# Performance work log

Hardware: AMD Instinct MI355X
Metric: run time of the kernel (lower is better)

## Reference

```python
import jax, jax.numpy as jnp
import numpy as np

B = 8192
D_IN = 2048
MM = 1600
CHUNKS = 20
CS = MM // CHUNKS  # 80
D_OUT = 3000
EPS = 1e-12  # F.normalize clamp eps


def setup_inputs() -> dict:
    key = jax.random.key(0)
    ks = jax.random.split(key, 10)
    s_in = 1.0 / np.sqrt(D_IN)
    s_c = 1.0 / np.sqrt(CS)
    s_mm = 1.0 / np.sqrt(MM)
    return {
        "x0": jax.random.normal(ks[0], (B, D_IN), jnp.float32),
        "x1": jax.random.normal(ks[1], (B, D_IN), jnp.float32),
        "W0": jax.random.uniform(ks[2], (D_IN, MM), jnp.float32, -s_in, s_in),
        "b0": jax.random.uniform(ks[3], (MM,), jnp.float32, -s_in, s_in),
        "W1": jax.random.uniform(ks[4], (D_IN, MM), jnp.float32, -s_in, s_in),
        "b1": jax.random.uniform(ks[5], (MM,), jnp.float32, -s_in, s_in),
        # stacked bilinear weights: [chunks, out, in1, in2] like torch Bilinear
        "Wb": jax.random.uniform(ks[6], (CHUNKS, CS, CS, CS), jnp.float32, -s_c, s_c),
        "bb": jax.random.uniform(ks[7], (CHUNKS, CS), jnp.float32, -s_c, s_c),
        "Wout": jax.random.uniform(ks[8], (MM, D_OUT), jnp.float32, -s_mm, s_mm),
        "bout": jax.random.uniform(ks[9], (D_OUT,), jnp.float32, -s_mm, s_mm),
    }


def reference(x0, x1, W0, b0, W1, b1, Wb, bb, Wout, bout):
    # input projections: [B, MM]
    h0 = x0 @ W0 + b0
    h1 = x1 @ W1 + b1
    # split into equal chunks: [B, CHUNKS, CS]
    h0c = h0.reshape(B, CHUNKS, CS)
    h1c = h1.reshape(B, CHUNKS, CS)
    # batched bilinear over all chunks: z[b,c,o] = sum_{s,t} h0[b,c,s] Wb[c,o,s,t] h1[b,c,t] + bb[c,o]
    z = jnp.einsum('bcs,cost,bct->bco', h0c, Wb, h1c) + bb[None, :, :]
    # signed sqrt (pos_norm == 'before_cat')
    z = jnp.sqrt(jax.nn.relu(z)) - jnp.sqrt(jax.nn.relu(-z))
    # L2 normalize per chunk (torch F.normalize over dim=1 of the [B, CS] chunk)
    norm = jnp.linalg.norm(z, axis=-1, keepdims=True)
    z = z / jnp.maximum(norm, EPS)
    # concat chunks -> [B, MM], final projection
    z = z.reshape(B, MM)
    return z @ Wout + bout
```

## Files before the change

kernel.cpp:

```cpp
#include <hip/hip_runtime.h>
#include <hip/hip_bf16.h>

typedef unsigned short u16;
typedef unsigned int   u32;

using bf16x8 = __attribute__((ext_vector_type(8))) short;
using f32x4  = __attribute__((ext_vector_type(4))) float;
using fvec4  = __attribute__((ext_vector_type(4))) float;
using u16x4  = __attribute__((ext_vector_type(4))) unsigned short;

#define BSZ   8192
#define DIN   2048
#define MMD   1600
#define NCH   20
#define CSZ   80
#define DOUT  3000

__device__ __forceinline__ float bf2f(u16 u) {
    u32 x = ((u32)u) << 16; float f; __builtin_memcpy(&f, &x, 4); return f;
}
__device__ __forceinline__ u16 f2bf(float f) {
    u32 x; __builtin_memcpy(&x, &f, 4);
    u32 r = x + 0x7fffu + ((x >> 16) & 1u);
    return (u16)(r >> 16);
}

__device__ __forceinline__ void gl2lds16(const void* g, const void* l) {
    __builtin_amdgcn_global_load_lds(
        (const __attribute__((address_space(1))) u32*)g,
        (__attribute__((address_space(3))) u32*)l, 16, 0, 0);
}

__global__ void cast_bf16_k(const float* __restrict__ src, u16* __restrict__ dst, int n4) {
    int i = blockIdx.x * blockDim.x + threadIdx.x;
    if (i < n4) {
        fvec4 v = ((const fvec4*)src)[i];
        u16x4 o;
        o.x = f2bf(v.x); o.y = f2bf(v.y); o.z = f2bf(v.z); o.w = f2bf(v.w);
        ((u16x4*)dst)[i] = o;
    }
}

__global__ void transpose_cast_k(const float* __restrict__ src, u16* __restrict__ dst,
                                 int K, int N) {
    __shared__ float t[32][33];
    int k0 = blockIdx.x * 32, n0 = blockIdx.y * 32;
    int tx = threadIdx.x & 31, ty = threadIdx.x >> 5;
#pragma unroll
    for (int r = 0; r < 4; r++) {
        int n = n0 + tx;
        float v = (n < N) ? src[(size_t)(k0 + ty + 8 * r) * N + n] : 0.f;
        t[ty + 8 * r][tx] = v;
    }
    __syncthreads();
#pragma unroll
    for (int r = 0; r < 4; r++)
        dst[(size_t)(n0 + ty + 8 * r) * K + k0 + tx] = f2bf(t[tx][ty + 8 * r]);
}

template<bool OUT_BF16>
__global__ __launch_bounds__(256, 2) void gemm_bt_k(
    const u16* __restrict__ A, const u16* __restrict__ BT,
    const float* __restrict__ bias, void* __restrict__ C, int K, int N) {
    __shared__ __align__(16) u16 As[128 * 64];
    __shared__ __align__(16) u16 Bs[128 * 64];
    const int tid = threadIdx.x, w = tid >> 6, lane = tid & 63;
    const int lr = lane & 15, lk = lane >> 4, s7 = lr & 7;
    const int m0 = blockIdx.x * 128, n0 = blockIdx.y * 128;
    const int mh = (w >> 1) * 64, nh = (w & 1) * 64;
    const int so = (lane & 7) ^ (lane >> 3);
    int arow[4], brow[4];
#pragma unroll
    for (int i = 0; i < 4; i++) { arow[i] = (mh + i * 16 + lr) * 64; brow[i] = (nh + i * 16 + lr) * 64; }
    f32x4 acc[4][4] = {};
    const u16* Ag = A + (size_t)m0 * K;
    const u16* Bg = BT + (size_t)n0 * K;
    const int nslab = K >> 6;
    for (int kt = 0; kt < nslab; ++kt) {
        const int k0 = kt * 64;
        __syncthreads();
#pragma unroll
        for (int q = 0; q < 4; q++) {
            int ch = w * 4 + q;
            int row = ch * 8 + (lane >> 3);
            gl2lds16(Ag + (size_t)row * K + k0 + so * 8, As + ch * 512);
            gl2lds16(Bg + (size_t)row * K + k0 + so * 8, Bs + ch * 512);
        }
        __syncthreads();
#pragma unroll
        for (int ks = 0; ks < 64; ks += 32) {
            const int px = (((ks >> 3) + lk) ^ s7) * 8;
            bf16x8 av[4], bv[4];
#pragma unroll
            for (int i = 0; i < 4; i++) av[i] = *(const bf16x8*)(As + arow[i] + px);
#pragma unroll
            for (int j = 0; j < 4; j++) bv[j] = *(const bf16x8*)(Bs + brow[j] + px);
#pragma unroll
            for (int i = 0; i < 4; i++)
#pragma unroll
                for (int j = 0; j < 4; j++)
                    acc[i][j] = __builtin_amdgcn_mfma_f32_16x16x32_bf16(av[i], bv[j], acc[i][j], 0, 0, 0);
        }
    }
#pragma unroll
    for (int j = 0; j < 4; j++) {
        int n = n0 + nh + j * 16 + lr;
        if (n < N) {
            float bv = bias[n];
#pragma unroll
            for (int i = 0; i < 4; i++) {
                int mb = m0 + mh + i * 16 + lk * 4;
#pragma unroll
                for (int r = 0; r < 4; r++) {
                    float v = acc[i][j][r] + bv;
                    if (OUT_BF16) ((u16*)C)[(size_t)(mb + r) * N + n] = f2bf(v);
                    else          ((float*)C)[(size_t)(mb + r) * N + n] = v;
                }
            }
        }
    }
}

__global__ __launch_bounds__(256, 2) void bilinear_k(
    const u16* __restrict__ h0g, const u16* __restrict__ h1g,
    const u16* __restrict__ Wbg, const float* __restrict__ bbg,
    u16* __restrict__ zg) {
    constexpr int WROW = 104;
    constexpr int WBUF = CSZ * WROW;
    __shared__ __align__(16) u16 Ws[3 * WBUF];
    const int tid = threadIdx.x, w = tid >> 6, lane = tid & 63;
    const int lr = lane & 15, lk = lane >> 4;
    const int m0 = blockIdx.x * 128, c = blockIdx.y;

#pragma unroll
    for (int t = 0; t < 2; ++t) {
        int q = t * 256 + tid;
        if (q < 480) {
            int b = q / 160, r2 = q - b * 160;
            *(fvec4*)(Ws + b * WBUF + (r2 >> 1) * WROW + 80 + (r2 & 1) * 8) =
                (fvec4){0.f, 0.f, 0.f, 0.f};
        }
    }

    const u16* WgBase = Wbg + (size_t)c * CSZ * 6400;
    const u16* wsrc[5];
    bool wok[5];
    int wdst[5];
#pragma unroll
    for (int it = 0; it < 5; ++it) {
        int p = it * 256 + tid;
        int row = p / 13, o = p - row * 13;
        wok[it] = (p < 1040) && (o < 10);
        wsrc[it] = WgBase + (size_t)row * 6400 + o * 8;
        wdst[it] = (it * 256 + w * 64) * 8;
    }

    const u16* hbase = h0g + (size_t)m0 * MMD + c * CSZ;
    int hoff[8];
#pragma unroll
    for (int i = 0; i < 2; ++i)
#pragma unroll
        for (int r = 0; r < 4; ++r)
            hoff[i * 4 + r] = (w * 32 + i * 16 + lk * 4 + r) * MMD;

#pragma unroll
    for (int it = 0; it < 5; ++it) {
        if (wok[it]) gl2lds16(wsrc[it], Ws + wdst[it]);
        wsrc[it] += CSZ;
    }
    u16 h0r[8];
#pragma unroll
    for (int k = 0; k < 8; ++k) h0r[k] = hbase[hoff[k]];
    const u16* hs = hbase + 1;

    bf16x8 av[2][3];
    const u16* h1base = h1g + (size_t)m0 * MMD + c * CSZ;
#pragma unroll
    for (int i = 0; i < 2; ++i) {
        const u16* rowp = h1base + (size_t)(w * 32 + i * 16 + lr) * MMD;
#pragma unroll
        for (int st = 0; st < 3; ++st) {
            if (st == 2 && lk >= 2) {
                av[i][st] = (bf16x8){0, 0, 0, 0, 0, 0, 0, 0};
            } else {
                av[i][st] = *(const bf16x8*)(rowp + st * 32 + lk * 8);
            }
        }
    }

    __syncthreads();

    int boff[5];
#pragma unroll
    for (int j = 0; j < 5; ++j) boff[j] = (j * 16 + lr) * WROW + lk * 8;

    f32x4 z[2][5] = {};
    const f32x4 zf = {0.f, 0.f, 0.f, 0.f};
    int bufR = 0, bufW = 1;
#pragma unroll 1
    for (int s = 0; s < 80; ++s) {
        u16 h0n[8];
        if (s < 79) {
#pragma unroll
            for (int it = 0; it < 5; ++it) {
                if (wok[it]) gl2lds16(wsrc[it], Ws + bufW * WBUF + wdst[it]);
                wsrc[it] += CSZ;
            }
#pragma unroll
            for (int k = 0; k < 8; ++k) h0n[k] = hs[hoff[k]];
            hs += 1;
            asm volatile("s_waitcnt vmcnt(12)" ::: "memory");
        } else {
            asm volatile("s_waitcnt vmcnt(0)" ::: "memory");
        }
        __builtin_amdgcn_s_barrier();
        asm volatile("" ::: "memory");

        const u16* Wr = Ws + bufR * WBUF;
        f32x4 P[2][5];
#pragma unroll
        for (int st = 0; st < 3; ++st) {
            bf16x8 bv[5];
#pragma unroll
            for (int j = 0; j < 5; ++j) bv[j] = *(const bf16x8*)(Wr + boff[j] + st * 32);
#pragma unroll
            for (int i = 0; i < 2; ++i)
#pragma unroll
                for (int j = 0; j < 5; ++j)
                    P[i][j] = __builtin_amdgcn_mfma_f32_16x16x32_bf16(
                        av[i][st], bv[j], st == 0 ? zf : P[i][j], 0, 0, 0);
        }
#pragma unroll
        for (int i = 0; i < 2; ++i)
#pragma unroll
            for (int r = 0; r < 4; ++r) {
                float h0f = bf2f(h0r[i * 4 + r]);
#pragma unroll
                for (int j = 0; j < 5; ++j)
                    z[i][j][r] += h0f * P[i][j][r];
            }
        if (s < 79) {
#pragma unroll
            for (int k = 0; k < 8; ++k) h0r[k] = h0n[k];
        }
        bufR = (bufR == 2) ? 0 : bufR + 1;
        bufW = (bufW == 2) ? 0 : bufW + 1;
    }

    float bbv[5];
#pragma unroll
    for (int j = 0; j < 5; j++) bbv[j] = bbg[c * CSZ + j * 16 + lr];
    float sq[2][4] = {};
#pragma unroll
    for (int i = 0; i < 2; i++)
#pragma unroll
        for (int j = 0; j < 5; j++)
#pragma unroll
            for (int r = 0; r < 4; r++) {
                float v = z[i][j][r] + bbv[j];
                float a = sqrtf(fabsf(v));
                v = (v < 0.f) ? -a : a;
                z[i][j][r] = v;
                sq[i][r] += v * v;
            }
#pragma unroll
    for (int d = 1; d < 16; d <<= 1)
#pragma unroll
        for (int i = 0; i < 2; i++)
#pragma unroll
            for (int r = 0; r < 4; r++)
                sq[i][r] += __shfl_xor(sq[i][r], d, 64);
    float sc[2][4];
#pragma unroll
    for (int i = 0; i < 2; i++)
#pragma unroll
        for (int r = 0; r < 4; r++)
            sc[i][r] = 1.f / fmaxf(sqrtf(sq[i][r]), 1e-12f);
#pragma unroll
    for (int i = 0; i < 2; i++)
#pragma unroll
        for (int r = 0; r < 4; r++) {
            int row = m0 + w * 32 + i * 16 + lk * 4 + r;
#pragma unroll
            for (int j = 0; j < 5; j++) {
                int col = c * CSZ + j * 16 + lr;
                zg[(size_t)row * MMD + col] = f2bf(z[i][j][r] * sc[i][r]);
            }
        }
}

extern "C" void kernel_launch(void* const* d_in, const int* in_sizes, int n_in,
                              void* d_out, int out_size, void* d_ws, size_t ws_size,
                              hipStream_t stream) {
    (void)in_sizes; (void)n_in; (void)out_size; (void)ws_size;
    const float* x0 = (const float*)d_in[0];
    const float* x1 = (const float*)d_in[1];
    const float* W0 = (const float*)d_in[2];
    const float* b0 = (const float*)d_in[3];
    const float* W1 = (const float*)d_in[4];
    const float* b1 = (const float*)d_in[5];
    const float* Wb = (const float*)d_in[6];
    const float* bb = (const float*)d_in[7];
    const float* Wo = (const float*)d_in[8];
    const float* bo = (const float*)d_in[9];

    char* ws = (char*)d_ws;
    size_t off = 0;
    auto alloc = [&](size_t bytes) { void* p = ws + off; off += (bytes + 255) & ~(size_t)255; return p; };
    u16* x0b = (u16*)alloc((size_t)BSZ * DIN * 2);
    u16* x1b = (u16*)alloc((size_t)BSZ * DIN * 2);
    u16* W0T = (u16*)alloc((size_t)1664 * DIN * 2);
    u16* W1T = (u16*)alloc((size_t)1664 * DIN * 2);
    u16* WbB = (u16*)alloc((size_t)NCH * CSZ * 6400 * 2);
    u16* WoT = (u16*)alloc((size_t)3072 * MMD * 2);
    u16* h0  = (u16*)alloc((size_t)BSZ * MMD * 2);
    u16* h1  = (u16*)alloc((size_t)BSZ * MMD * 2);
    u16* z   = x0b;

    cast_bf16_k<<<dim3(16384), dim3(256), 0, stream>>>(x0, x0b, (BSZ * DIN) / 4);
    cast_bf16_k<<<dim3(16384), dim3(256), 0, stream>>>(x1, x1b, (BSZ * DIN) / 4);
    cast_bf16_k<<<dim3(10000), dim3(256), 0, stream>>>(Wb, WbB, (NCH * CSZ * 6400) / 4);
    transpose_cast_k<<<dim3(DIN / 32, 1664 / 32), dim3(256), 0, stream>>>(W0, W0T, DIN, MMD);
    transpose_cast_k<<<dim3(DIN / 32, 1664 / 32), dim3(256), 0, stream>>>(W1, W1T, DIN, MMD);
    transpose_cast_k<<<dim3(MMD / 32, 3072 / 32), dim3(256), 0, stream>>>(Wo, WoT, MMD, DOUT);
    gemm_bt_k<true><<<dim3(BSZ / 128, 13), dim3(256), 0, stream>>>(x0b, W0T, b0, h0, DIN, MMD);
    gemm_bt_k<true><<<dim3(BSZ / 128, 13), dim3(256), 0, stream>>>(x1b, W1T, b1, h1, DIN, MMD);
    bilinear_k<<<dim3(BSZ / 128, NCH), dim3(256), 0, stream>>>(h0, h1, WbB, bb, z);
    gemm_bt_k<false><<<dim3(BSZ / 128, 24), dim3(256), 0, stream>>>(z, WoT, bo, d_out, MMD, DOUT);
}
```

Measured before the change: 731.1 us.

## Double bilinear row tile to 256 per block to reuse staged Wb slices

Each bilinear block now covers 256 batch rows (64 per wave) instead of 128, so every Wb slice staged into LDS feeds twice as many MFMAs and the grid halves. The inner loop is unrolled by two with ping-pong h0 register buffers, which removes the per-step register copy. The MFMA work is split into 3+2 output column groups so the partial-product registers stay bounded. The larger tile raises register pressure and halves the number of blocks, which may cut occupancy and leave CUs less evenly loaded.

```diff
diff --git a/kernel.cpp b/kernel.cpp
--- a/kernel.cpp
+++ b/kernel.cpp
@@ -128,16 +128,17 @@
     constexpr int WROW = 104;
     constexpr int WBUF = CSZ * WROW;
     __shared__ __align__(16) u16 Ws[3 * WBUF];
+    u16* Wsm = Ws;
     const int tid = threadIdx.x, w = tid >> 6, lane = tid & 63;
     const int lr = lane & 15, lk = lane >> 4;
-    const int m0 = blockIdx.x * 128, c = blockIdx.y;
+    const int m0 = blockIdx.x * 256, c = blockIdx.y;
 
 #pragma unroll
     for (int t = 0; t < 2; ++t) {
         int q = t * 256 + tid;
         if (q < 480) {
             int b = q / 160, r2 = q - b * 160;
-            *(fvec4*)(Ws + b * WBUF + (r2 >> 1) * WROW + 80 + (r2 & 1) * 8) =
+            *(fvec4*)(Wsm + b * WBUF + (r2 >> 1) * WROW + 80 + (r2 & 1) * 8) =
                 (fvec4){0.f, 0.f, 0.f, 0.f};
         }
     }
@@ -148,36 +149,20 @@
     int wdst[5];
 #pragma unroll
     for (int it = 0; it < 5; ++it) {
-        int p = it * 256 + tid;
+        int p, dstoct;
+        if (it < 4) { p = it * 256 + tid;        dstoct = it * 256 + w * 64; }
+        else        { p = 1024 + w * 4 + lane;   dstoct = 1024 + w * 4;      }
         int row = p / 13, o = p - row * 13;
-        wok[it] = (p < 1040) && (o < 10);
+        wok[it] = (o < 10) && (it < 4 || lane < 4);
         wsrc[it] = WgBase + (size_t)row * 6400 + o * 8;
-        wdst[it] = (it * 256 + w * 64) * 8;
-    }
-
-    const u16* hbase = h0g + (size_t)m0 * MMD + c * CSZ;
-    int hoff[8];
-#pragma unroll
-    for (int i = 0; i < 2; ++i)
-#pragma unroll
-        for (int r = 0; r < 4; ++r)
-            hoff[i * 4 + r] = (w * 32 + i * 16 + lk * 4 + r) * MMD;
-
-#pragma unroll
-    for (int it = 0; it < 5; ++it) {
-        if (wok[it]) gl2lds16(wsrc[it], Ws + wdst[it]);
-        wsrc[it] += CSZ;
-    }
-    u16 h0r[8];
-#pragma unroll
-    for (int k = 0; k < 8; ++k) h0r[k] = hbase[hoff[k]];
-    const u16* hs = hbase + 1;
-
-    bf16x8 av[2][3];
+        wdst[it] = dstoct * 8;
+    }
+
+    bf16x8 av[4][3];
     const u16* h1base = h1g + (size_t)m0 * MMD + c * CSZ;
 #pragma unroll
-    for (int i = 0; i < 2; ++i) {
-        const u16* rowp = h1base + (size_t)(w * 32 + i * 16 + lr) * MMD;
+    for (int i = 0; i < 4; ++i) {
+        const u16* rowp = h1base + (size_t)(w * 64 + i * 16 + lr) * MMD;
 #pragma unroll
         for (int st = 0; st < 3; ++st) {
             if (st == 2 && lk >= 2) {
@@ -188,71 +173,112 @@
         }
     }
 
+    const u16* hb[16];
+#pragma unroll
+    for (int i = 0; i < 4; ++i)
+#pragma unroll
+        for (int r = 0; r < 4; ++r)
+            hb[i * 4 + r] = h0g + (size_t)(m0 + i * 16 + r) * MMD + c * CSZ;
+    const int voff = (w * 64 + lk * 4) * MMD;
+
+#pragma unroll
+    for (int it = 0; it < 5; ++it) {
+        if (wok[it]) gl2lds16(wsrc[it], Wsm + wdst[it]);
+        wsrc[it] += CSZ;
+    }
+    u16 h0a[16], h0b[16];
+#pragma unroll
+    for (int k = 0; k < 16; ++k) h0a[k] = hb[k][voff];
+
     __syncthreads();
 
     int boff[5];
 #pragma unroll
     for (int j = 0; j < 5; ++j) boff[j] = (j * 16 + lr) * WROW + lk * 8;
 
-    f32x4 z[2][5] = {};
+    f32x4 z[4][5] = {};
     const f32x4 zf = {0.f, 0.f, 0.f, 0.f};
-    int bufR = 0, bufW = 1;
+    int bufR = 0;
+
+#define BILIN_ITER(S, HU, HL)                                               \
+    {                                                                       \
+        if ((S) < 79) {                                                     \
+            u16* wWp = Wsm + ((bufR + 1 == 3) ? 0 : bufR + 1) * WBUF;       \
+            _Pragma("unroll")                                               \
+            for (int it = 0; it < 5; ++it) {                                \
+                if (wok[it]) gl2lds16(wsrc[it], wWp + wdst[it]);            \
+                wsrc[it] += CSZ;                                            \
+            }                                                               \
+            _Pragma("unroll")                                               \
+            for (int k = 0; k < 16; ++k) HL[k] = hb[k][voff + (S) + 1];     \
+            asm volatile("s_waitcnt vmcnt(21)" ::: "memory");               \
+        } else {                                                            \
+            asm volatile("s_waitcnt vmcnt(0)" ::: "memory");                \
+        }                                                                   \
+        __builtin_amdgcn_s_barrier();                                       \
+        asm volatile("" ::: "memory");                                      \
+        const u16* Wr = Wsm + bufR * WBUF;                                  \
+        f32x4 P[4][3];                                                      \
+        _Pragma("unroll")                                                   \
+        for (int st = 0; st < 3; ++st) {                                    \
+            bf16x8 bv[3];                                                   \
+            _Pragma("unroll")                                               \
+            for (int jj = 0; jj < 3; ++jj)                                  \
+                bv[jj] = *(const bf16x8*)(Wr + boff[jj] + st * 32);         \
+            _Pragma("unroll")                                               \
+            for (int i = 0; i < 4; ++i)                                     \
+                _Pragma("unroll")                                           \
+                for (int jj = 0; jj < 3; ++jj)                              \
+                    P[i][jj] = __builtin_amdgcn_mfma_f32_16x16x32_bf16(     \
+                        av[i][st], bv[jj], st == 0 ? zf : P[i][jj], 0, 0, 0); \
+        }                                                                   \
+        _Pragma("unroll")                                                   \
+        for (int i = 0; i < 4; ++i)                                         \
+            _Pragma("unroll")                                               \
+            for (int r = 0; r < 4; ++r) {                                   \
+                float h0f = bf2f(HU[i * 4 + r]);                            \
+                _Pragma("unroll")                                           \
+                for (int jj = 0; jj < 3; ++jj)                              \
+                    z[i][jj][r] += h0f * P[i][jj][r];                       \
+            }                                                               \
+        _Pragma("unroll")                                                   \
+        for (int st = 0; st < 3; ++st) {                                    \
+            bf16x8 bv[2];                                                   \
+            _Pragma("unroll")                                               \
+            for (int jj = 0; jj < 2; ++jj)                                  \
+                bv[jj] = *(const bf16x8*)(Wr + boff[3 + jj] + st * 32);     \
+            _Pragma("unroll")                                               \
+            for (int i = 0; i < 4; ++i)                                     \
+                _Pragma("unroll")                                           \
+                for (int jj = 0; jj < 2; ++jj)                              \
+                    P[i][jj] = __builtin_amdgcn_mfma_f32_16x16x32_bf16(     \
+                        av[i][st], bv[jj], st == 0 ? zf : P[i][jj], 0, 0, 0); \
+        }                                                                   \
+        _Pragma("unroll")                                                   \
+        for (int i = 0; i < 4; ++i)                                         \
+            _Pragma("unroll")                                               \
+            for (int r = 0; r < 4; ++r) {                                   \
+                float h0f = bf2f(HU[i * 4 + r]);                            \
+                _Pragma("unroll")                                           \
+                for (int jj = 0; jj < 2; ++jj)                              \
+                    z[i][3 + jj][r] += h0f * P[i][jj][r];                   \
+            }                                                               \
+        bufR = (bufR == 2) ? 0 : bufR + 1;                                  \
+    }
+
 #pragma unroll 1
-    for (int s = 0; s < 80; ++s) {
-        u16 h0n[8];
-        if (s < 79) {
-#pragma unroll
-            for (int it = 0; it < 5; ++it) {
-                if (wok[it]) gl2lds16(wsrc[it], Ws + bufW * WBUF + wdst[it]);
-                wsrc[it] += CSZ;
-            }
-#pragma unroll
-            for (int k = 0; k < 8; ++k) h0n[k] = hs[hoff[k]];
-            hs += 1;
-            asm volatile("s_waitcnt vmcnt(12)" ::: "memory");
-        } else {
-            asm volatile("s_waitcnt vmcnt(0)" ::: "memory");
-        }
-        __builtin_amdgcn_s_barrier();
-        asm volatile("" ::: "memory");
-
-        const u16* Wr = Ws + bufR * WBUF;
-        f32x4 P[2][5];
-#pragma unroll
-        for (int st = 0; st < 3; ++st) {
-            bf16x8 bv[5];
-#pragma unroll
-            for (int j = 0; j < 5; ++j) bv[j] = *(const bf16x8*)(Wr + boff[j] + st * 32);
-#pragma unroll
-            for (int i = 0; i < 2; ++i)
-#pragma unroll
-                for (int j = 0; j < 5; ++j)
-                    P[i][j] = __builtin_amdgcn_mfma_f32_16x16x32_bf16(
-                        av[i][st], bv[j], st == 0 ? zf : P[i][j], 0, 0, 0);
-        }
-#pragma unroll
-        for (int i = 0; i < 2; ++i)
-#pragma unroll
-            for (int r = 0; r < 4; ++r) {
-                float h0f = bf2f(h0r[i * 4 + r]);
-#pragma unroll
-                for (int j = 0; j < 5; ++j)
-                    z[i][j][r] += h0f * P[i][j][r];
-            }
-        if (s < 79) {
-#pragma unroll
-            for (int k = 0; k < 8; ++k) h0r[k] = h0n[k];
-        }
-        bufR = (bufR == 2) ? 0 : bufR + 1;
-        bufW = (bufW == 2) ? 0 : bufW + 1;
-    }
+    for (int s2 = 0; s2 < 80; s2 += 2) {
+        BILIN_ITER(s2,     h0a, h0b)
+        BILIN_ITER(s2 + 1, h0b, h0a)
+    }
+#undef BILIN_ITER
 
     float bbv[5];
 #pragma unroll
     for (int j = 0; j < 5; j++) bbv[j] = bbg[c * CSZ + j * 16 + lr];
-    float sq[2][4] = {};
-#pragma unroll
-    for (int i = 0; i < 2; i++)
+    float sq[4][4] = {};
+#pragma unroll
+    for (int i = 0; i < 4; i++)
 #pragma unroll
         for (int j = 0; j < 5; j++)
 #pragma unroll
@@ -266,21 +292,21 @@
 #pragma unroll
     for (int d = 1; d < 16; d <<= 1)
 #pragma unroll
-        for (int i = 0; i < 2; i++)
+        for (int i = 0; i < 4; i++)
 #pragma unroll
             for (int r = 0; r < 4; r++)
                 sq[i][r] += __shfl_xor(sq[i][r], d, 64);
-    float sc[2][4];
-#pragma unroll
-    for (int i = 0; i < 2; i++)
+    float sc[4][4];
+#pragma unroll
+    for (int i = 0; i < 4; i++)
 #pragma unroll
         for (int r = 0; r < 4; r++)
             sc[i][r] = 1.f / fmaxf(sqrtf(sq[i][r]), 1e-12f);
 #pragma unroll
-    for (int i = 0; i < 2; i++)
+    for (int i = 0; i < 4; i++)
 #pragma unroll
         for (int r = 0; r < 4; r++) {
-            int row = m0 + w * 32 + i * 16 + lk * 4 + r;
+            int row = m0 + w * 64 + i * 16 + lk * 4 + r;
 #pragma unroll
             for (int j = 0; j < 5; j++) {
                 int col = c * CSZ + j * 16 + lr;
@@ -325,6 +351,6 @@
     transpose_cast_k<<<dim3(MMD / 32, 3072 / 32), dim3(256), 0, stream>>>(Wo, WoT, MMD, DOUT);
     gemm_bt_k<true><<<dim3(BSZ / 128, 13), dim3(256), 0, stream>>>(x0b, W0T, b0, h0, DIN, MMD);
     gemm_bt_k<true><<<dim3(BSZ / 128, 13), dim3(256), 0, stream>>>(x1b, W1T, b1, h1, DIN, MMD);
-    bilinear_k<<<dim3(BSZ / 128, NCH), dim3(256), 0, stream>>>(h0, h1, WbB, bb, z);
+    bilinear_k<<<dim3(BSZ / 256, NCH), dim3(256), 0, stream>>>(h0, h1, WbB, bb, z);
     gemm_bt_k<false><<<dim3(BSZ / 128, 24), dim3(256), 0, stream>>>(z, WoT, bo, d_out, MMD, DOUT);
 }
```

After: 1.175 ms. +60.7%, slower.
